# Kernel tuning notes

Hardware: AMD Instinct MI355X
Metric: run time of the kernel (lower is better)

The kernel has to match this reference:

```python
import jax, jax.numpy as jnp
import numpy as np

N, H, W, C, K = 8, 512, 512, 3, 5
PAD = K // 2  # odd square kernel, 'same' zero padding


def setup_inputs() -> dict:
    key = jax.random.key(0)
    k1, k2 = jax.random.split(key)
    input_data = jax.random.normal(k1, (N, H, W, C), dtype=jnp.float32)
    # per-sample, per-pixel unshared kernels: (N, H, W, K*K)
    weights = jax.random.normal(k2, (N, H, W, K * K), dtype=jnp.float32) * 0.1
    return {"input_data": input_data, "weights": weights}


def reference(input_data, weights):
    # Local (untied) depthwise conv: out[n,h,w,c] =
    #   sum_{dh,dw} in[n, h+dh-P, w+dw-P, c] * weights[n, h, w, dh*K+dw]
    # Weight is shared across channels (no channel dim in weights).
    x = jnp.pad(input_data, ((0, 0), (PAD, PAD), (PAD, PAD), (0, 0)))
    out = jnp.zeros_like(input_data)
    for k in range(K * K):  # fixed small loop over kernel taps
        dh, dw = k // K, k % K
        out = out + x[:, dh:dh + H, dw:dw + W, :] * weights[..., k:k + 1]
    return out
```

## Files before the change

kernel.cpp:

```cpp
#include <hip/hip_runtime.h>

#define NN 8
#define HH 512
#define WW 512
#define CC 3
#define KK 5
#define PADP 2
#define WROWF (WW * CC)
#define NBLOCKS 4096

typedef float f4a __attribute__((ext_vector_type(4), aligned(4)));

struct Row { f4a L0, L1, L2, L3; };

__device__ __forceinline__ void load_row(const float* rb, Row& r) {
    r.L0 = *(const f4a*)(rb);
    r.L1 = *(const f4a*)(rb + 4);
    r.L2 = *(const f4a*)(rb + 8);
    r.L3 = *(const f4a*)(rb + 11);
}

__device__ __forceinline__ void fma_row(const Row& r, const float* wp,
                                        float& a0, float& a1, float& a2) {
    const float w0 = wp[0], w1 = wp[1], w2 = wp[2], w3 = wp[3], w4 = wp[4];
    a0 = fmaf(r.L0[0], w0, a0); a1 = fmaf(r.L0[1], w0, a1); a2 = fmaf(r.L0[2], w0, a2);
    a0 = fmaf(r.L0[3], w1, a0); a1 = fmaf(r.L1[0], w1, a1); a2 = fmaf(r.L1[1], w1, a2);
    a0 = fmaf(r.L1[2], w2, a0); a1 = fmaf(r.L1[3], w2, a1); a2 = fmaf(r.L2[0], w2, a2);
    a0 = fmaf(r.L2[1], w3, a0); a1 = fmaf(r.L2[2], w3, a1); a2 = fmaf(r.L2[3], w3, a2);
    a0 = fmaf(r.L3[1], w4, a0); a1 = fmaf(r.L3[2], w4, a1); a2 = fmaf(r.L3[3], w4, a2);
}

#define GLDS16(gp, lp) __builtin_amdgcn_global_load_lds( \
    (const __attribute__((address_space(1))) void*)(gp), \
    (__attribute__((address_space(3))) void*)(lp), 16, 0, 0)
#define GLDS4(gp, lp) __builtin_amdgcn_global_load_lds( \
    (const __attribute__((address_space(1))) void*)(gp), \
    (__attribute__((address_space(3))) void*)(lp), 4, 0, 0)

__global__ __launch_bounds__(64, 4) void conv_local_kernel(
    const float* __restrict__ in,
    const float* __restrict__ wt,
    float* __restrict__ out)
{
    __shared__ float wldsA[64 * KK * KK];
    __shared__ float wldsB[64 * KK * KK];

    const int lane = threadIdx.x;
    const int b    = ((blockIdx.x & 7) << 9) | (blockIdx.x >> 3);
    const int n    = b >> 9;
    const int rem  = b & 511;
    const int hp   = rem >> 1;
    const int half = rem & 1;
    const int h0   = hp << 1;
    const int nHH  = n * HH;

    const float* inb  = in + (size_t)n * (HH * WW * CC);
    const bool  rowok = (hp >= 1) && (hp <= 254);

#pragma unroll 1
    for (int j = 0; j < 4; ++j) {
        const int  w0 = (((half << 2) | j)) << 6;
        const long p0 = (long)(nHH + h0) * WW + w0;
        const long p1 = p0 + WW;

        asm volatile("s_waitcnt lgkmcnt(0)" ::: "memory");

        {
            const char* s0 = (const char*)(wt + p0 * (KK * KK));
            const char* s1 = (const char*)(wt + p1 * (KK * KK));
#pragma unroll
            for (int it = 0; it < 6; ++it)
                GLDS16(s0 + it * 1024 + lane * 16, wldsA + it * 256);
            GLDS4(s0 + 6144 + lane * 4, wldsA + 1536);
#pragma unroll
            for (int it = 0; it < 6; ++it)
                GLDS16(s1 + it * 1024 + lane * 16, wldsB + it * 256);
            GLDS4(s1 + 6144 + lane * 4, wldsB + 1536);
        }

        const float* wp0 = &wldsA[lane * (KK * KK)];
        const float* wp1 = &wldsB[lane * (KK * KK)];
        const bool fast = rowok && (w0 != 0) && (w0 != WW - 64);

        if (fast) {
            const float* rb = inb + ((long)(h0 - PADP) * WW + (w0 + lane - PADP)) * CC;
            Row R0, R1, R2, R3, R4, R5;
            load_row(rb + 0 * WROWF, R0);
            load_row(rb + 1 * WROWF, R1);
            load_row(rb + 2 * WROWF, R2);
            load_row(rb + 3 * WROWF, R3);
            load_row(rb + 4 * WROWF, R4);
            load_row(rb + 5 * WROWF, R5);
            asm volatile("s_waitcnt vmcnt(0)" ::: "memory");
            __builtin_amdgcn_sched_barrier(0);

            float a0 = 0.f, a1 = 0.f, a2 = 0.f;
            float c0 = 0.f, c1 = 0.f, c2 = 0.f;
            fma_row(R0, wp0 + 0,  a0, a1, a2);
            fma_row(R1, wp0 + 5,  a0, a1, a2);
            fma_row(R1, wp1 + 0,  c0, c1, c2);
            fma_row(R2, wp0 + 10, a0, a1, a2);
            fma_row(R2, wp1 + 5,  c0, c1, c2);
            fma_row(R3, wp0 + 15, a0, a1, a2);
            fma_row(R3, wp1 + 10, c0, c1, c2);
            fma_row(R4, wp0 + 20, a0, a1, a2);
            fma_row(R4, wp1 + 15, c0, c1, c2);
            fma_row(R5, wp1 + 20, c0, c1, c2);

            float* o0 = out + (p0 + lane) * CC;
            o0[0] = a0; o0[1] = a1; o0[2] = a2;
            float* o1 = out + (p1 + lane) * CC;
            o1[0] = c0; o1[1] = c1; o1[2] = c2;
        } else {
            asm volatile("s_waitcnt vmcnt(0)" ::: "memory");
            __builtin_amdgcn_sched_barrier(0);
#pragma unroll
            for (int px = 0; px < 2; ++px) {
                const int hh = h0 + px;
                const int w  = w0 + lane;
                const float* wp = px ? wp1 : wp0;
                float a0 = 0.f, a1 = 0.f, a2 = 0.f;
#pragma unroll
                for (int dh = 0; dh < KK; ++dh) {
                    const int ih = hh + dh - PADP;
                    const bool rok = ((unsigned)ih < (unsigned)HH);
#pragma unroll
                    for (int dw = 0; dw < KK; ++dw) {
                        const int iw = w + dw - PADP;
                        const bool ok = rok && ((unsigned)iw < (unsigned)WW);
                        const float* p = inb + ((long)(ih * WW + iw)) * CC;
                        float v0 = ok ? p[0] : 0.f;
                        float v1 = ok ? p[1] : 0.f;
                        float v2 = ok ? p[2] : 0.f;
                        const float wv = wp[dh * KK + dw];
                        a0 = fmaf(v0, wv, a0);
                        a1 = fmaf(v1, wv, a1);
                        a2 = fmaf(v2, wv, a2);
                    }
                }
                float* o = out + ((long)(nHH + hh) * WW + w) * CC;
                o[0] = a0; o[1] = a1; o[2] = a2;
            }
        }
    }
}

extern "C" void kernel_launch(void* const* d_in, const int* in_sizes, int n_in,
                              void* d_out, int out_size, void* d_ws, size_t ws_size,
                              hipStream_t stream) {
    const float* in = (const float*)d_in[0];
    const float* wt = (const float*)d_in[1];
    float* out = (float*)d_out;

    conv_local_kernel<<<NBLOCKS, 64, 0, stream>>>(in, wt, out);
}
```

Baseline: 56.39 us.

## Double-buffer LDS weight staging to prefetch next tile during compute

Adds a second pair of LDS buffers so the per-pixel weights for the next column tile are fetched with global_load_lds while the current tile's input rows load and its FMAs run. A partial vmcnt wait replaces the full drain, so only the current stage and row loads must finish. This doubles LDS use per block, which may lower the number of resident blocks per CU. The kernel is already close to bandwidth-bound, so the room to gain is small.

```diff
diff --git a/kernel.cpp b/kernel.cpp
--- a/kernel.cpp
+++ b/kernel.cpp
@@ -37,13 +37,32 @@
     (const __attribute__((address_space(1))) void*)(gp), \
     (__attribute__((address_space(3))) void*)(lp), 4, 0, 0)
 
+#define STAGE2(d0, d1, jj) do {                                          \
+    const long _p = (long)(nHH + h0) * WW + (((half << 2) | (jj)) << 6); \
+    const char* _s0 = (const char*)(wt + _p * (KK * KK));                \
+    const char* _s1 = (const char*)(wt + (_p + WW) * (KK * KK));         \
+    _Pragma("unroll")                                                    \
+    for (int _it = 0; _it < 6; ++_it)                                    \
+        GLDS16(_s0 + _it * 1024 + lane * 16, (d0) + _it * 256);          \
+    GLDS4(_s0 + 6144 + lane * 4, (d0) + 1536);                           \
+    _Pragma("unroll")                                                    \
+    for (int _it = 0; _it < 6; ++_it)                                    \
+        GLDS16(_s1 + _it * 1024 + lane * 16, (d1) + _it * 256);          \
+    GLDS4(_s1 + 6144 + lane * 4, (d1) + 1536);                           \
+} while (0)
+
+#define WAITK(N) do {                                                    \
+    asm volatile("s_waitcnt vmcnt(" #N ")" ::: "memory");                \
+    __builtin_amdgcn_sched_barrier(0);                                   \
+} while (0)
+
 __global__ __launch_bounds__(64, 4) void conv_local_kernel(
     const float* __restrict__ in,
     const float* __restrict__ wt,
     float* __restrict__ out)
 {
-    __shared__ float wldsA[64 * KK * KK];
-    __shared__ float wldsB[64 * KK * KK];
+    __shared__ float bA0[1600], bA1[1600];
+    __shared__ float bB0[1600], bB1[1600];
 
     const int lane = threadIdx.x;
     const int b    = ((blockIdx.x & 7) << 9) | (blockIdx.x >> 3);
@@ -57,63 +76,57 @@
     const float* inb  = in + (size_t)n * (HH * WW * CC);
     const bool  rowok = (hp >= 1) && (hp <= 254);
 
+    float* c0 = bA0; float* c1 = bA1;
+    float* n0 = bB0; float* n1 = bB1;
+
+    STAGE2(c0, c1, 0);
+
 #pragma unroll 1
     for (int j = 0; j < 4; ++j) {
         const int  w0 = (((half << 2) | j)) << 6;
         const long p0 = (long)(nHH + h0) * WW + w0;
         const long p1 = p0 + WW;
+        const bool wfast = rowok && (w0 != 0) && (w0 != WW - 64);
 
-        asm volatile("s_waitcnt lgkmcnt(0)" ::: "memory");
-
-        {
-            const char* s0 = (const char*)(wt + p0 * (KK * KK));
-            const char* s1 = (const char*)(wt + p1 * (KK * KK));
-#pragma unroll
-            for (int it = 0; it < 6; ++it)
-                GLDS16(s0 + it * 1024 + lane * 16, wldsA + it * 256);
-            GLDS4(s0 + 6144 + lane * 4, wldsA + 1536);
-#pragma unroll
-            for (int it = 0; it < 6; ++it)
-                GLDS16(s1 + it * 1024 + lane * 16, wldsB + it * 256);
-            GLDS4(s1 + 6144 + lane * 4, wldsB + 1536);
-        }
-
-        const float* wp0 = &wldsA[lane * (KK * KK)];
-        const float* wp1 = &wldsB[lane * (KK * KK)];
-        const bool fast = rowok && (w0 != 0) && (w0 != WW - 64);
-
-        if (fast) {
+        Row R0, R1, R2, R3, R4, R5;
+        if (wfast) {
             const float* rb = inb + ((long)(h0 - PADP) * WW + (w0 + lane - PADP)) * CC;
-            Row R0, R1, R2, R3, R4, R5;
             load_row(rb + 0 * WROWF, R0);
             load_row(rb + 1 * WROWF, R1);
             load_row(rb + 2 * WROWF, R2);
             load_row(rb + 3 * WROWF, R3);
             load_row(rb + 4 * WROWF, R4);
             load_row(rb + 5 * WROWF, R5);
-            asm volatile("s_waitcnt vmcnt(0)" ::: "memory");
-            __builtin_amdgcn_sched_barrier(0);
+        }
+        if (j < 3) {
+            STAGE2(n0, n1, j + 1);
+            WAITK(14);
+        } else {
+            WAITK(0);
+        }
 
+        const float* wp0 = &c0[lane * (KK * KK)];
+        const float* wp1 = &c1[lane * (KK * KK)];
+
+        if (wfast) {
             float a0 = 0.f, a1 = 0.f, a2 = 0.f;
-            float c0 = 0.f, c1 = 0.f, c2 = 0.f;
+            float d0 = 0.f, d1 = 0.f, d2 = 0.f;
             fma_row(R0, wp0 + 0,  a0, a1, a2);
             fma_row(R1, wp0 + 5,  a0, a1, a2);
-            fma_row(R1, wp1 + 0,  c0, c1, c2);
+            fma_row(R1, wp1 + 0,  d0, d1, d2);
             fma_row(R2, wp0 + 10, a0, a1, a2);
-            fma_row(R2, wp1 + 5,  c0, c1, c2);
+            fma_row(R2, wp1 + 5,  d0, d1, d2);
             fma_row(R3, wp0 + 15, a0, a1, a2);
-            fma_row(R3, wp1 + 10, c0, c1, c2);
+            fma_row(R3, wp1 + 10, d0, d1, d2);
             fma_row(R4, wp0 + 20, a0, a1, a2);
-            fma_row(R4, wp1 + 15, c0, c1, c2);
-            fma_row(R5, wp1 + 20, c0, c1, c2);
+            fma_row(R4, wp1 + 15, d0, d1, d2);
+            fma_row(R5, wp1 + 20, d0, d1, d2);
 
             float* o0 = out + (p0 + lane) * CC;
             o0[0] = a0; o0[1] = a1; o0[2] = a2;
             float* o1 = out + (p1 + lane) * CC;
-            o1[0] = c0; o1[1] = c1; o1[2] = c2;
+            o1[0] = d0; o1[1] = d1; o1[2] = d2;
         } else {
-            asm volatile("s_waitcnt vmcnt(0)" ::: "memory");
-            __builtin_amdgcn_sched_barrier(0);
 #pragma unroll
             for (int px = 0; px < 2; ++px) {
                 const int hh = h0 + px;
@@ -142,6 +155,10 @@
                 o[0] = a0; o[1] = a1; o[2] = a2;
             }
         }
+
+        float* t;
+        t = c0; c0 = n0; n0 = t;
+        t = c1; c1 = n1; n1 = t;
     }
 }
 
```

Measured after the change: 63.13 us. 1.12x slower.

## Process one output row per block and prefetch next weight tile

Applied to the files above, without the earlier changes.

Each block now handles a single output row instead of a pair of rows, and the grid doubles to compensate. The shared weight buffer shrinks to one, and the next chunk's weights are staged right after the current chunk's compute so their load overlaps the following input loads. This gives up the vertical input reuse of the two-row scheme, which loaded 6 rows for 2 outputs, for lower LDS use, fewer live registers and more blocks in flight. The prefetch also shares the same vmcnt wait as the input loads, so weight and input latency are now coupled.

```diff
diff --git a/kernel.cpp b/kernel.cpp
--- a/kernel.cpp
+++ b/kernel.cpp
@@ -7,7 +7,7 @@
 #define KK 5
 #define PADP 2
 #define WROWF (WW * CC)
-#define NBLOCKS 4096
+#define NBLOCKS 8192
 
 typedef float f4a __attribute__((ext_vector_type(4), aligned(4)));
 
@@ -37,110 +37,101 @@
     (const __attribute__((address_space(1))) void*)(gp), \
     (__attribute__((address_space(3))) void*)(lp), 4, 0, 0)
 
+#define STAGE(jj) do {                                                  \
+    const long _p = rowpix + (((half << 2) | (jj)) << 6);               \
+    const char* _s = (const char*)(wt + _p * (KK * KK));                \
+    _Pragma("unroll")                                                   \
+    for (int _it = 0; _it < 6; ++_it)                                   \
+        GLDS16(_s + _it * 1024 + lane * 16, wbuf + _it * 256);          \
+    GLDS4(_s + 6144 + lane * 4, wbuf + 1536);                          \
+} while (0)
+
+#define WAITV0() do {                                                   \
+    asm volatile("s_waitcnt vmcnt(0)" ::: "memory");                    \
+    __builtin_amdgcn_sched_barrier(0);                                  \
+} while (0)
+
+#define LGKM0() do {                                                    \
+    asm volatile("s_waitcnt lgkmcnt(0)" ::: "memory");                  \
+    __builtin_amdgcn_sched_barrier(0);                                  \
+} while (0)
+
 __global__ __launch_bounds__(64, 4) void conv_local_kernel(
     const float* __restrict__ in,
     const float* __restrict__ wt,
     float* __restrict__ out)
 {
-    __shared__ float wldsA[64 * KK * KK];
-    __shared__ float wldsB[64 * KK * KK];
+    __shared__ float wbuf[64 * KK * KK];
 
     const int lane = threadIdx.x;
-    const int b    = ((blockIdx.x & 7) << 9) | (blockIdx.x >> 3);
-    const int n    = b >> 9;
-    const int rem  = b & 511;
-    const int hp   = rem >> 1;
+    const int b    = ((blockIdx.x & 7) << 10) | (blockIdx.x >> 3);
+    const int n    = b >> 10;
+    const int rem  = b & 1023;
+    const int h    = rem >> 1;
     const int half = rem & 1;
-    const int h0   = hp << 1;
-    const int nHH  = n * HH;
+    const long rowpix = (long)(n * HH + h) * WW;
 
     const float* inb  = in + (size_t)n * (HH * WW * CC);
-    const bool  rowok = (hp >= 1) && (hp <= 254);
+    const bool  rowok = (h >= PADP) && (h < HH - PADP);
+
+    STAGE(0);
 
 #pragma unroll 1
     for (int j = 0; j < 4; ++j) {
         const int  w0 = (((half << 2) | j)) << 6;
-        const long p0 = (long)(nHH + h0) * WW + w0;
-        const long p1 = p0 + WW;
+        const long p0 = rowpix + w0;
+        const bool wfast = rowok && (w0 != 0) && (w0 != WW - 64);
 
-        asm volatile("s_waitcnt lgkmcnt(0)" ::: "memory");
-
-        {
-            const char* s0 = (const char*)(wt + p0 * (KK * KK));
-            const char* s1 = (const char*)(wt + p1 * (KK * KK));
-#pragma unroll
-            for (int it = 0; it < 6; ++it)
-                GLDS16(s0 + it * 1024 + lane * 16, wldsA + it * 256);
-            GLDS4(s0 + 6144 + lane * 4, wldsA + 1536);
-#pragma unroll
-            for (int it = 0; it < 6; ++it)
-                GLDS16(s1 + it * 1024 + lane * 16, wldsB + it * 256);
-            GLDS4(s1 + 6144 + lane * 4, wldsB + 1536);
-        }
-
-        const float* wp0 = &wldsA[lane * (KK * KK)];
-        const float* wp1 = &wldsB[lane * (KK * KK)];
-        const bool fast = rowok && (w0 != 0) && (w0 != WW - 64);
-
-        if (fast) {
-            const float* rb = inb + ((long)(h0 - PADP) * WW + (w0 + lane - PADP)) * CC;
-            Row R0, R1, R2, R3, R4, R5;
+        if (wfast) {
+            const float* rb = inb + ((long)(h - PADP) * WW + (w0 + lane - PADP)) * CC;
+            Row R0, R1, R2, R3, R4;
             load_row(rb + 0 * WROWF, R0);
             load_row(rb + 1 * WROWF, R1);
             load_row(rb + 2 * WROWF, R2);
             load_row(rb + 3 * WROWF, R3);
             load_row(rb + 4 * WROWF, R4);
-            load_row(rb + 5 * WROWF, R5);
-            asm volatile("s_waitcnt vmcnt(0)" ::: "memory");
-            __builtin_amdgcn_sched_barrier(0);
+            WAITV0();
 
+            const float* wp = &wbuf[lane * (KK * KK)];
             float a0 = 0.f, a1 = 0.f, a2 = 0.f;
-            float c0 = 0.f, c1 = 0.f, c2 = 0.f;
-            fma_row(R0, wp0 + 0,  a0, a1, a2);
-            fma_row(R1, wp0 + 5,  a0, a1, a2);
-            fma_row(R1, wp1 + 0,  c0, c1, c2);
-            fma_row(R2, wp0 + 10, a0, a1, a2);
-            fma_row(R2, wp1 + 5,  c0, c1, c2);
-            fma_row(R3, wp0 + 15, a0, a1, a2);
-            fma_row(R3, wp1 + 10, c0, c1, c2);
-            fma_row(R4, wp0 + 20, a0, a1, a2);
-            fma_row(R4, wp1 + 15, c0, c1, c2);
-            fma_row(R5, wp1 + 20, c0, c1, c2);
+            fma_row(R0, wp + 0,  a0, a1, a2);
+            fma_row(R1, wp + 5,  a0, a1, a2);
+            fma_row(R2, wp + 10, a0, a1, a2);
+            fma_row(R3, wp + 15, a0, a1, a2);
+            fma_row(R4, wp + 20, a0, a1, a2);
 
-            float* o0 = out + (p0 + lane) * CC;
-            o0[0] = a0; o0[1] = a1; o0[2] = a2;
-            float* o1 = out + (p1 + lane) * CC;
-            o1[0] = c0; o1[1] = c1; o1[2] = c2;
+            float* o = out + (p0 + lane) * CC;
+            o[0] = a0; o[1] = a1; o[2] = a2;
         } else {
-            asm volatile("s_waitcnt vmcnt(0)" ::: "memory");
-            __builtin_amdgcn_sched_barrier(0);
+            WAITV0();
+            const float* wp = &wbuf[lane * (KK * KK)];
+            const int w = w0 + lane;
+            float a0 = 0.f, a1 = 0.f, a2 = 0.f;
 #pragma unroll
-            for (int px = 0; px < 2; ++px) {
-                const int hh = h0 + px;
-                const int w  = w0 + lane;
-                const float* wp = px ? wp1 : wp0;
-                float a0 = 0.f, a1 = 0.f, a2 = 0.f;
+            for (int dh = 0; dh < KK; ++dh) {
+                const int ih = h + dh - PADP;
+                const bool rok = ((unsigned)ih < (unsigned)HH);
 #pragma unroll
-                for (int dh = 0; dh < KK; ++dh) {
-                    const int ih = hh + dh - PADP;
-                    const bool rok = ((unsigned)ih < (unsigned)HH);
-#pragma unroll
-                    for (int dw = 0; dw < KK; ++dw) {
-                        const int iw = w + dw - PADP;
-                        const bool ok = rok && ((unsigned)iw < (unsigned)WW);
-                        const float* p = inb + ((long)(ih * WW + iw)) * CC;
-                        float v0 = ok ? p[0] : 0.f;
-                        float v1 = ok ? p[1] : 0.f;
-                        float v2 = ok ? p[2] : 0.f;
-                        const float wv = wp[dh * KK + dw];
-                        a0 = fmaf(v0, wv, a0);
-                        a1 = fmaf(v1, wv, a1);
-                        a2 = fmaf(v2, wv, a2);
-                    }
+                for (int dw = 0; dw < KK; ++dw) {
+                    const int iw = w + dw - PADP;
+                    const bool ok = rok && ((unsigned)iw < (unsigned)WW);
+                    const float* p = inb + ((long)(ih * WW + iw)) * CC;
+                    float v0 = ok ? p[0] : 0.f;
+                    float v1 = ok ? p[1] : 0.f;
+                    float v2 = ok ? p[2] : 0.f;
+                    const float wv = wp[dh * KK + dw];
+                    a0 = fmaf(v0, wv, a0);
+                    a1 = fmaf(v1, wv, a1);
+                    a2 = fmaf(v2, wv, a2);
                 }
-                float* o = out + ((long)(nHH + hh) * WW + w) * CC;
-                o[0] = a0; o[1] = a1; o[2] = a2;
             }
+            float* o = out + (p0 + lane) * CC;
+            o[0] = a0; o[1] = a1; o[2] = a2;
+        }
+
+        if (j < 3) {
+            LGKM0();
+            STAGE(j + 1);
         }
     }
 }
```

Result: slower. 60.23 us (+6.8%).
